# Kernel optimization log

Hardware: AMD Instinct MI355X
Metric: run time of the kernel (lower is better)

Reference implementation:

```python
import jax, jax.numpy as jnp
import numpy as np
import math

EMBED_DIM = 1024
NUM_HEADS = 16
HEAD_DIM = EMBED_DIM // NUM_HEADS


def setup_inputs() -> dict:
    key = jax.random.key(0)
    ks = jax.random.split(key, 5)
    x = jax.random.normal(ks[0], (4, 2048, EMBED_DIM), dtype=jnp.float32)
    # Linear params (torch nn.Linear: y = x @ W.T + b); init scale ~ 1/sqrt(fan_in)
    s = 1.0 / math.sqrt(EMBED_DIM)
    qkv_w = jax.random.uniform(ks[1], (3 * EMBED_DIM, EMBED_DIM), jnp.float32, -s, s)
    qkv_b = jax.random.uniform(ks[2], (3 * EMBED_DIM,), jnp.float32, -s, s)
    proj_w = jax.random.uniform(ks[3], (EMBED_DIM, EMBED_DIM), jnp.float32, -s, s)
    proj_b = jax.random.uniform(ks[4], (EMBED_DIM,), jnp.float32, -s, s)
    return {"x": x, "qkv_w": qkv_w, "qkv_b": qkv_b, "proj_w": proj_w, "proj_b": proj_b}


def reference(x, qkv_w, qkv_b, proj_w, proj_b):
    bsz, num_tokens, dim = x.shape
    qkv = x @ qkv_w.T + qkv_b  # [B, S, 3*D]
    qkv = qkv.reshape(bsz, num_tokens, 3, NUM_HEADS, HEAD_DIM)
    qkv = jnp.transpose(qkv, (2, 0, 3, 1, 4))  # [3, B, H, S, hd]
    q, k, v = qkv[0], qkv[1], qkv[2]
    scale = 1.0 / math.sqrt(HEAD_DIM)
    attn_scores = jnp.einsum('bhqd,bhkd->bhqk', q, k) * scale  # [B, H, S, S]
    attn = jax.nn.softmax(attn_scores, axis=-1)
    out = jnp.einsum('bhqk,bhkd->bhqd', attn, v)  # [B, H, S, hd]
    out = jnp.transpose(out, (0, 2, 1, 3)).reshape(bsz, num_tokens, dim)
    out = out @ proj_w.T + proj_b
    return out
```

## Files before the change

### kernel.cpp

```cpp
#include <hip/hip_runtime.h>
#include <stdint.h>

#define DEVICE static __device__ __forceinline__

typedef __bf16 bf16x8 __attribute__((ext_vector_type(8)));
typedef float f32x4 __attribute__((ext_vector_type(4)));

#define AS1 __attribute__((address_space(1)))
#define AS3 __attribute__((address_space(3)))

DEVICE void g2l16(const void* gptr, void* lptr) {
  __builtin_amdgcn_global_load_lds((AS1 uint32_t*)(uintptr_t)gptr,
                                   (AS3 uint32_t*)(uint32_t)(uintptr_t)lptr,
                                   16, 0, 0);
}

DEVICE float b2f(ushort h) {
  union { uint32_t u; float f; } v;
  v.u = ((uint32_t)h) << 16;
  return v.f;
}
DEVICE ushort f2b(float f) {
  union { float f; uint32_t u; } v;
  v.f = f;
  uint32_t u = v.u;
  return (ushort)((u + 0x7FFFu + ((u >> 16) & 1u)) >> 16);
}

#if defined(__has_builtin) && __has_builtin(__builtin_amdgcn_exp2f)
DEVICE float fast_exp2(float x) { return __builtin_amdgcn_exp2f(x); }
#else
extern "C" __device__ float __ocml_native_exp2_f32(float);
DEVICE float fast_exp2(float x) { return __ocml_native_exp2_f32(x); }
#endif

#define QSCALE 0.1803368801111244f

DEVICE int kperm(int x) {
  return (x & 0x23) | ((x & 0x18) >> 1) | ((x & 0x4) << 2);
}

__global__ void detect_dtype(const ushort* __restrict__ xu, int* __restrict__ flag) {
  __shared__ int bad;
  if (threadIdx.x == 0) bad = 0;
  __syncthreads();
  int mybad = 0;
#pragma unroll
  for (int j = 0; j < 8; ++j) {
    const int i = threadIdx.x * 8 + j;
    const ushort u = xu[2 * i];
    const int e = (u >> 7) & 0xFF;
    if (!(e == 0 || (e >= 96 && e <= 160))) mybad++;
  }
  atomicAdd(&bad, mybad);
  __syncthreads();
  if (threadIdx.x == 0) *flag = (bad > 512) ? 1 : 0;
}

__global__ void convert_bf16(const void* __restrict__ src, ushort* __restrict__ dst,
                             int n, const int* __restrict__ flag) {
  const bool isf32 = (*flag != 0);
  const int n8 = n >> 3;
  for (int i = blockIdx.x * blockDim.x + threadIdx.x; i < n8;
       i += gridDim.x * blockDim.x) {
    ushort pk[8];
    if (isf32) {
      const float4 a = ((const float4*)src)[2 * i];
      const float4 b = ((const float4*)src)[2 * i + 1];
      pk[0] = f2b(a.x); pk[1] = f2b(a.y); pk[2] = f2b(a.z); pk[3] = f2b(a.w);
      pk[4] = f2b(b.x); pk[5] = f2b(b.y); pk[6] = f2b(b.z); pk[7] = f2b(b.w);
      *(uint4*)&dst[8 * i] = *(const uint4*)pk;
    } else {
      *(uint4*)&dst[8 * i] = ((const uint4*)src)[i];
    }
  }
}

template <int MODE>
__global__ __launch_bounds__(256)
void gemm_bt(const ushort* __restrict__ A, const ushort* __restrict__ W,
             const ushort* __restrict__ bias, ushort* __restrict__ O0,
             ushort* __restrict__ O1, ushort* __restrict__ O2,
             int M, int N, int K, const int* __restrict__ flag)
{
  __shared__ union SM {
    struct { ushort As[128 * 64]; ushort Bs[128 * 64]; } s;
    ushort Ct[128 * 136];
  } sm;

  const int tid = threadIdx.x;
  const int lane = tid & 63;
  const int wave = tid >> 6;
  const int quad = lane >> 4;
  const int lo = lane & 15;
  const int m0 = blockIdx.y * 128;
  const int n0 = blockIdx.x * 128;
  const int wm = (wave >> 1) * 64;
  const int wn = (wave & 1) * 64;

  f32x4 acc[4][4] = {};

  for (int k0 = 0; k0 < K; k0 += 64) {
    __syncthreads();
#pragma unroll
    for (int i = 0; i < 4; ++i) {
      const int c = tid + 256 * i;
      const int row = c >> 3;
      const int kc = (c & 7) << 3;
      g2l16(A + (size_t)(m0 + row) * K + k0 + kc,
            (char*)sm.s.As + ((wave << 6) + (i << 8)) * 16);
      g2l16(W + (size_t)(n0 + row) * K + k0 + kc,
            (char*)sm.s.Bs + ((wave << 6) + (i << 8)) * 16);
    }
    __syncthreads();

#pragma unroll
    for (int ks = 0; ks < 2; ++ks) {
      bf16x8 af[4], bfr[4];
#pragma unroll
      for (int t = 0; t < 4; ++t) {
        af[t]  = *(const bf16x8*)&sm.s.As[(wm + t * 16 + lo) * 64 + ks * 32 + quad * 8];
        bfr[t] = *(const bf16x8*)&sm.s.Bs[(wn + t * 16 + lo) * 64 + ks * 32 + quad * 8];
      }
#pragma unroll
      for (int mt = 0; mt < 4; ++mt)
#pragma unroll
        for (int nt = 0; nt < 4; ++nt)
          acc[mt][nt] = __builtin_amdgcn_mfma_f32_16x16x32_bf16(
              af[mt], bfr[nt], acc[mt][nt], 0, 0, 0);
    }
  }

  if (MODE == 0) {
    const int which = n0 >> 10;
    if (which == 2) {
#pragma unroll
      for (int nt = 0; nt < 4; ++nt) {
        const int n = n0 + wn + nt * 16 + lo;
        const float bv2 = b2f(bias[n]);
        const int h = (n >> 6) & 15;
        const int d = n & 63;
#pragma unroll
        for (int mt = 0; mt < 4; ++mt) {
          const int mb = m0 + wm + mt * 16 + quad * 4;
          const int b = mb >> 11, s0 = mb & 2047;
          ushort pk[4];
#pragma unroll
          for (int r = 0; r < 4; ++r) pk[r] = f2b(acc[mt][nt][r] + bv2);
          *(uint2*)&O2[((size_t)(b * 16 + h) * 64 + d) * 2048 + s0] =
              *(const uint2*)pk;
        }
      }
    } else {
      const float qs = (which == 0) ? QSCALE : 1.0f;
      ushort* __restrict__ dst = (which == 0) ? O0 : O1;
      __syncthreads();
#pragma unroll
      for (int nt = 0; nt < 4; ++nt) {
        const int n = n0 + wn + nt * 16 + lo;
        const float bv2 = b2f(bias[n]);
#pragma unroll
        for (int mt = 0; mt < 4; ++mt)
#pragma unroll
          for (int r = 0; r < 4; ++r)
            sm.Ct[(wm + mt * 16 + quad * 4 + r) * 136 + wn + nt * 16 + lo] =
                f2b((acc[mt][nt][r] + bv2) * qs);
      }
      __syncthreads();
#pragma unroll
      for (int i = 0; i < 8; ++i) {
        const int c = tid + 256 * i;
        const int nch = c & 15;
        const int ml = c >> 4;
        const int n = n0 + nch * 8;
        const int h = (n >> 6) & 15;
        const int d = n & 63;
        const int mg = m0 + ml;
        const int b = mg >> 11;
        int s = mg & 2047;
        if (which == 1) s = (s & ~63) | kperm(s & 63);
        const uint4 val = *(const uint4*)&sm.Ct[ml * 136 + nch * 8];
        *(uint4*)&dst[(((size_t)(b * 16 + h) * 2048 + s) << 6) + d] = val;
      }
    }
  } else {
    const bool f32out = (*flag != 0);
    float* Of = (float*)O0;
#pragma unroll
    for (int nt = 0; nt < 4; ++nt) {
      const int n = n0 + wn + nt * 16 + lo;
      const float bv2 = b2f(bias[n]);
#pragma unroll
      for (int mt = 0; mt < 4; ++mt)
#pragma unroll
        for (int r = 0; r < 4; ++r) {
          const int m = m0 + wm + mt * 16 + quad * 4 + r;
          const float val = acc[mt][nt][r] + bv2;
          if (f32out) Of[(size_t)m * N + n] = val;
          else        O0[(size_t)m * N + n] = f2b(val);
        }
    }
  }
}

__global__ __launch_bounds__(256)
void attn_fwd(const ushort* __restrict__ qp, const ushort* __restrict__ kp,
              const ushort* __restrict__ vp, ushort* __restrict__ o)
{
  __shared__ ushort Qs[128 * 64];
  __shared__ ushort Ks[64 * 64];
  __shared__ ushort Vt[64 * 64];

  const int tid = threadIdx.x;
  const int lane = tid & 63;
  const int wave = tid >> 6;
  const int quad = lane >> 4;
  const int lo = lane & 15;
  const int bh = blockIdx.y;
  const int q0 = blockIdx.x * 128;

  const ushort* Qg = qp + (size_t)bh * 2048 * 64;
  const ushort* Kg = kp + (size_t)bh * 2048 * 64;
  const ushort* Vg = vp + (size_t)bh * 64 * 2048;

#pragma unroll
  for (int i = 0; i < 4; ++i) {
    const int c = tid + 256 * i;
    const int row = c >> 3;
    const int kc = (c & 7) << 3;
    g2l16(Qg + (size_t)(q0 + row) * 64 + kc,
          (char*)Qs + ((wave << 6) + (i << 8)) * 16);
  }
  __syncthreads();

  bf16x8 qf[2][2];
#pragma unroll
  for (int mt = 0; mt < 2; ++mt)
#pragma unroll
    for (int ks = 0; ks < 2; ++ks)
      qf[mt][ks] = *(const bf16x8*)&Qs[(wave * 32 + mt * 16 + lo) * 64 + ks * 32 + quad * 8];

  f32x4 oacc[2][4] = {};
  float lrow[2] = {0.0f, 0.0f};

  for (int j0 = 0; j0 < 2048; j0 += 64) {
    __syncthreads();
#pragma unroll
    for (int i = 0; i < 2; ++i) {
      const int c = tid + 256 * i;
      const int row = c >> 3;
      const int kc = (c & 7) << 3;
      g2l16(Kg + (size_t)(j0 + row) * 64 + kc,
            (char*)Ks + ((wave << 6) + (i << 8)) * 16);
      g2l16(Vg + (size_t)row * 2048 + j0 + kc,
            (char*)Vt + ((wave << 6) + (i << 8)) * 16);
    }
    __syncthreads();

    f32x4 sacc[2][4] = {};
#pragma unroll
    for (int ks = 0; ks < 2; ++ks) {
#pragma unroll
      for (int nt = 0; nt < 4; ++nt) {
        const bf16x8 kf = *(const bf16x8*)&Ks[(nt * 16 + lo) * 64 + ks * 32 + quad * 8];
#pragma unroll
        for (int mt = 0; mt < 2; ++mt)
          sacc[mt][nt] = __builtin_amdgcn_mfma_f32_16x16x32_bf16(
              kf, qf[mt][ks], sacc[mt][nt], 0, 0, 0);
      }
    }

    bf16x8 pfr[2][2];
#pragma unroll
    for (int mt = 0; mt < 2; ++mt) {
      float rs = 0.0f;
      float p[4][4];
#pragma unroll
      for (int nt = 0; nt < 4; ++nt)
#pragma unroll
        for (int r = 0; r < 4; ++r) {
          p[nt][r] = fast_exp2(sacc[mt][nt][r]);
          rs += p[nt][r];
        }
      rs += __shfl_xor(rs, 16, 64);
      rs += __shfl_xor(rs, 32, 64);
      lrow[mt] += rs;
#pragma unroll
      for (int b = 0; b < 2; ++b)
#pragma unroll
        for (int h = 0; h < 2; ++h)
#pragma unroll
          for (int r = 0; r < 4; ++r)
            pfr[mt][b][4 * h + r] = (__bf16)p[2 * b + h][r];
    }

#pragma unroll
    for (int b = 0; b < 2; ++b) {
#pragma unroll
      for (int dt = 0; dt < 4; ++dt) {
        const bf16x8 vf = *(const bf16x8*)&Vt[(dt * 16 + lo) * 64 + b * 32 + quad * 8];
#pragma unroll
        for (int mt = 0; mt < 2; ++mt)
          oacc[mt][dt] = __builtin_amdgcn_mfma_f32_16x16x32_bf16(
              pfr[mt][b], vf, oacc[mt][dt], 0, 0, 0);
      }
    }
  }

  const int b_ = bh >> 4;
  const int h = bh & 15;
#pragma unroll
  for (int mt = 0; mt < 2; ++mt) {
#pragma unroll
    for (int r = 0; r < 4; ++r) {
      const float lr = __shfl(lrow[mt], quad * 4 + r, 64);
      const float inv = 1.0f / lr;
      const int srow = q0 + wave * 32 + mt * 16 + quad * 4 + r;
#pragma unroll
      for (int dt = 0; dt < 4; ++dt) {
        o[(((size_t)(b_ * 2048 + srow)) << 10) + h * 64 + dt * 16 + lo] =
            f2b(oacc[mt][dt][r] * inv);
      }
    }
  }
}

extern "C" void kernel_launch(void* const* d_in, const int* in_sizes, int n_in,
                              void* d_out, int out_size, void* d_ws, size_t ws_size,
                              hipStream_t stream) {
  const size_t N_X  = (size_t)4 * 2048 * 1024;
  const size_t N_WQ = (size_t)3072 * 1024;
  const size_t N_BQ = 3072;
  const size_t N_WP = (size_t)1024 * 1024;
  const size_t N_BP = 1024;
  const size_t HSD  = (size_t)64 * 2048 * 64;

  ushort* xb = (ushort*)d_ws;
  ushort* wq = xb + N_X;
  ushort* bq = wq + N_WQ;
  ushort* wp = bq + N_BQ;
  ushort* bp = wp + N_WP;
  ushort* qb = bp + N_BP;
  ushort* kb = qb + HSD;
  ushort* vb = kb + HSD;
  ushort* ab = vb + HSD;
  int* flag  = (int*)(ab + HSD);

  detect_dtype<<<1, 256, 0, stream>>>((const ushort*)d_in[0], flag);
  convert_bf16<<<1024, 256, 0, stream>>>(d_in[0], xb, (int)N_X, flag);
  convert_bf16<<<512, 256, 0, stream>>>(d_in[1], wq, (int)N_WQ, flag);
  convert_bf16<<<2, 256, 0, stream>>>(d_in[2], bq, (int)N_BQ, flag);
  convert_bf16<<<256, 256, 0, stream>>>(d_in[3], wp, (int)N_WP, flag);
  convert_bf16<<<1, 256, 0, stream>>>(d_in[4], bp, (int)N_BP, flag);

  gemm_bt<0><<<dim3(24, 64), dim3(256), 0, stream>>>(
      xb, wq, bq, qb, kb, vb, 8192, 3072, 1024, flag);
  attn_fwd<<<dim3(16, 64), dim3(256), 0, stream>>>(qb, kb, vb, ab);
  gemm_bt<1><<<dim3(8, 64), dim3(256), 0, stream>>>(
      ab, wp, bp, (ushort*)d_out, nullptr, nullptr, 8192, 1024, 1024, flag);
}
```

Baseline: 325.7 us.

## Group GEMM tile order, compute softmax row sums via MFMA, raise attention occupancy

The GEMM kernels now remap block indices into column groups (GN tiles wide) so that concurrently running blocks share weight tiles in L2. In attention, the per-row softmax denominator is accumulated by an extra MFMA against a vector of ones instead of scalar adds and cross-lane shuffles, which takes VALU and shuffle work off the critical path. Attention launch bounds now request 4 blocks per SM. The ones-MFMA adds matrix-core work and sums bf16-rounded probabilities, and the occupancy hint may force register spills.

After: 299.3 us. -8.1%, faster.

```diff
diff --git a/kernel.cpp b/kernel.cpp
--- a/kernel.cpp
+++ b/kernel.cpp
@@ -76,7 +76,7 @@
   }
 }
 
-template <int MODE>
+template <int MODE, int GN>
 __global__ __launch_bounds__(256)
 void gemm_bt(const ushort* __restrict__ A, const ushort* __restrict__ W,
              const ushort* __restrict__ bias, ushort* __restrict__ O0,
@@ -93,8 +93,16 @@
   const int wave = tid >> 6;
   const int quad = lane >> 4;
   const int lo = lane & 15;
-  const int m0 = blockIdx.y * 128;
-  const int n0 = blockIdx.x * 128;
+
+  const int lin = blockIdx.y * gridDim.x + blockIdx.x;
+  const int per = GN * gridDim.y;
+  const int grp = lin / per;
+  const int w   = lin % per;
+  const int bxn = grp * GN + (w % GN);
+  const int bym = w / GN;
+  const int m0 = bym * 128;
+  const int n0 = bxn * 128;
+
   const int wm = (wave >> 1) * 64;
   const int wn = (wave & 1) * 64;
 
@@ -203,7 +211,7 @@
   }
 }
 
-__global__ __launch_bounds__(256)
+__global__ __launch_bounds__(256, 4)
 void attn_fwd(const ushort* __restrict__ qp, const ushort* __restrict__ kp,
               const ushort* __restrict__ vp, ushort* __restrict__ o)
 {
@@ -240,8 +248,12 @@
     for (int ks = 0; ks < 2; ++ks)
       qf[mt][ks] = *(const bf16x8*)&Qs[(wave * 32 + mt * 16 + lo) * 64 + ks * 32 + quad * 8];
 
+  bf16x8 ones;
+#pragma unroll
+  for (int j = 0; j < 8; ++j) ones[j] = (__bf16)1.0f;
+
   f32x4 oacc[2][4] = {};
-  float lrow[2] = {0.0f, 0.0f};
+  f32x4 sumacc[2] = {};
 
   for (int j0 = 0; j0 < 2048; j0 += 64) {
     __syncthreads();
@@ -273,18 +285,12 @@
     bf16x8 pfr[2][2];
 #pragma unroll
     for (int mt = 0; mt < 2; ++mt) {
-      float rs = 0.0f;
       float p[4][4];
 #pragma unroll
       for (int nt = 0; nt < 4; ++nt)
 #pragma unroll
-        for (int r = 0; r < 4; ++r) {
+        for (int r = 0; r < 4; ++r)
           p[nt][r] = fast_exp2(sacc[mt][nt][r]);
-          rs += p[nt][r];
-        }
-      rs += __shfl_xor(rs, 16, 64);
-      rs += __shfl_xor(rs, 32, 64);
-      lrow[mt] += rs;
 #pragma unroll
       for (int b = 0; b < 2; ++b)
 #pragma unroll
@@ -296,6 +302,10 @@
 
 #pragma unroll
     for (int b = 0; b < 2; ++b) {
+#pragma unroll
+      for (int mt = 0; mt < 2; ++mt)
+        sumacc[mt] = __builtin_amdgcn_mfma_f32_16x16x32_bf16(
+            pfr[mt][b], ones, sumacc[mt], 0, 0, 0);
 #pragma unroll
       for (int dt = 0; dt < 4; ++dt) {
         const bf16x8 vf = *(const bf16x8*)&Vt[(dt * 16 + lo) * 64 + b * 32 + quad * 8];
@@ -313,8 +323,7 @@
   for (int mt = 0; mt < 2; ++mt) {
 #pragma unroll
     for (int r = 0; r < 4; ++r) {
-      const float lr = __shfl(lrow[mt], quad * 4 + r, 64);
-      const float inv = 1.0f / lr;
+      const float inv = 1.0f / sumacc[mt][r];
       const int srow = q0 + wave * 32 + mt * 16 + quad * 4 + r;
 #pragma unroll
       for (int dt = 0; dt < 4; ++dt) {
@@ -353,9 +362,9 @@
   convert_bf16<<<256, 256, 0, stream>>>(d_in[3], wp, (int)N_WP, flag);
   convert_bf16<<<1, 256, 0, stream>>>(d_in[4], bp, (int)N_BP, flag);
 
-  gemm_bt<0><<<dim3(24, 64), dim3(256), 0, stream>>>(
+  gemm_bt<0, 6><<<dim3(24, 64), dim3(256), 0, stream>>>(
       xb, wq, bq, qb, kb, vb, 8192, 3072, 1024, flag);
   attn_fwd<<<dim3(16, 64), dim3(256), 0, stream>>>(qb, kb, vb, ab);
-  gemm_bt<1><<<dim3(8, 64), dim3(256), 0, stream>>>(
+  gemm_bt<1, 4><<<dim3(8, 64), dim3(256), 0, stream>>>(
       ab, wp, bp, (ushort*)d_out, nullptr, nullptr, 8192, 1024, 1024, flag);
 }
```
